# Optimization experiments

Measured on AMD Instinct MI355X. Metric: run time of the kernel, lower is better.

The kernel has to match this reference:

```python
import jax, jax.numpy as jnp
import numpy as np

K_RATIO = 0.7  # initial_ratio at epoch 0

def setup_inputs() -> dict:
    key = jax.random.key(0)
    k1, k2, k3 = jax.random.split(key, 3)
    B, D, C = 65536, 512, 1000
    features = jax.random.normal(k1, (B, D), dtype=jnp.float32)
    targets = jax.random.randint(k2, (B,), 0, C, dtype=jnp.int64)
    W = jax.random.normal(k3, (D, C), dtype=jnp.float32) / np.sqrt(D)
    b = jnp.zeros((C,), dtype=jnp.float32)
    return {"features": features, "targets": targets, "W": W, "b": b}

def reference(features, targets, W, b):
    # model: linear classifier -> logits [B, C]
    logits = features @ W + b
    # per-sample cross-entropy (reduction='none')
    logp = jax.nn.log_softmax(logits, axis=-1)
    losses = -jnp.take_along_axis(logp, targets[:, None], axis=-1)[:, 0]  # [B]
    B = features.shape[0]
    num_ohem = int(B * K_RATIO)
    # top-k hard examples, mean of their losses
    top_vals, _ = jax.lax.top_k(losses, num_ohem)
    return top_vals.mean()
```

## Files before the change

### kernel.cpp

```cpp
#include <hip/hip_runtime.h>
#include <hip/hip_bf16.h>

#define BTOT 65536
#define DDIM 512
#define CDIM 1000
#define KSEL 45875

#define L2E 1.44269504088896340736f
#define LN2 0.69314718055994530942f
#define NEG_BIG -1.0e30f

typedef __attribute__((ext_vector_type(8))) short short8;
typedef __attribute__((ext_vector_type(8))) unsigned short ushort8;
typedef __attribute__((ext_vector_type(4))) float f32x4;

__device__ __forceinline__ unsigned short f2bf(float f) {
  unsigned u = __float_as_uint(f);
  u += 0x7FFFu + ((u >> 16) & 1u);
  return (unsigned short)(u >> 16);
}

__device__ __forceinline__ void gload_lds16(const void* g, void* l) {
  __builtin_amdgcn_global_load_lds(
      (const __attribute__((address_space(1))) unsigned int*)g,
      (__attribute__((address_space(3))) unsigned int*)l, 16, 0, 0);
}

__global__ void prep_wt(const float* __restrict__ W, unsigned short* __restrict__ Wg) {
  const int idx = blockIdx.x * 256 + threadIdx.x;
  const int c  = idx & 1023;
  const int k8 = idx >> 10;
  const int nc = c >> 5, cc = c & 31;
  ushort8 v;
#pragma unroll
  for (int j = 0; j < 8; ++j) {
    const int k = k8 * 8 + j;
    v[j] = (c < CDIM) ? f2bf(W[k * CDIM + c]) : (unsigned short)0;
  }
  const unsigned dst = (unsigned)nc * 32768u +
      (((((unsigned)cc) << 10) | (((unsigned)k8) << 4)) ^ ((((unsigned)cc) & 7u) << 4));
  *(ushort8*)((char*)Wg + dst) = v;
}

__global__ void prep_bias(const float* __restrict__ b, float* __restrict__ bp) {
  const int i = blockIdx.x * 256 + threadIdx.x;
  bp[i] = (i < CDIM) ? b[i] * L2E : NEG_BIG;
}

__global__ void zero_hist(unsigned* __restrict__ h) {
  ((uint4*)h)[blockIdx.x * 256 + threadIdx.x] = (uint4){0, 0, 0, 0};
}

__launch_bounds__(256, 2)
__global__ void ohem_losses(const float* __restrict__ feat,
                            const int* __restrict__ targets,
                            const unsigned short* __restrict__ Wg,
                            const float* __restrict__ bpad,
                            float* __restrict__ losses,
                            unsigned* __restrict__ histHi) {
  __shared__ unsigned char lbuf[2][32768];
  const int tid  = threadIdx.x;
  const int lane = tid & 63;
  const int wave = (blockIdx.x << 2) + (tid >> 6);
  const int rowB = wave << 5;
  const int l15  = lane & 15;
  const int lgrp = lane >> 4;

#pragma unroll
  for (int r = 0; r < 8; ++r) {
    const int off = (r * 256 + tid) * 16;
    gload_lds16((const char*)Wg + off, &lbuf[0][off]);
  }

  short8 a[2][16];
#pragma unroll
  for (int rf = 0; rf < 2; ++rf) {
    const float* src = feat + (size_t)(rowB + rf * 16 + l15) * DDIM + lgrp * 8;
#pragma unroll
    for (int ks = 0; ks < 16; ++ks) {
      const float4 f0 = *(const float4*)(src + ks * 32);
      const float4 f1 = *(const float4*)(src + ks * 32 + 4);
      short8 v;
      v[0] = (short)f2bf(f0.x); v[1] = (short)f2bf(f0.y);
      v[2] = (short)f2bf(f0.z); v[3] = (short)f2bf(f0.w);
      v[4] = (short)f2bf(f1.x); v[5] = (short)f2bf(f1.y);
      v[6] = (short)f2bf(f1.z); v[7] = (short)f2bf(f1.w);
      a[rf][ks] = v;
    }
  }

  int   tcol[8];
  float s[8], tv[8];
#pragma unroll
  for (int rf = 0; rf < 2; ++rf)
#pragma unroll
    for (int r = 0; r < 4; ++r) {
      const int slot = rf * 4 + r;
      tcol[slot] = targets[rowB + rf * 16 + lgrp * 4 + r];
      s[slot] = 0.f; tv[slot] = NEG_BIG;
    }

  __syncthreads();

  const unsigned xm    = ((unsigned)(l15 & 7)) << 4;
  const unsigned base0 = (((unsigned)l15) << 10) | (((unsigned)lgrp) << 4);
  const unsigned base1 = base0 + (16u << 10);

  for (int nc = 0; nc < 32; ++nc) {
    const int cur = nc & 1;
    if (nc + 1 < 32) {
      const char* src = (const char*)Wg + (size_t)(nc + 1) * 32768;
#pragma unroll
      for (int r = 0; r < 8; ++r) {
        const int off = (r * 256 + tid) * 16;
        gload_lds16(src + off, &lbuf[cur ^ 1][off]);
      }
    }

    f32x4 acc[2][2];
#pragma unroll
    for (int rf = 0; rf < 2; ++rf)
#pragma unroll
      for (int cf = 0; cf < 2; ++cf) acc[rf][cf] = (f32x4){0.f, 0.f, 0.f, 0.f};

    const unsigned char* lb = &lbuf[cur][0];
#pragma unroll
    for (int ks = 0; ks < 16; ++ks) {
      const unsigned o0 = (base0 | (((unsigned)ks) << 6)) ^ xm;
      const unsigned o1 = (base1 | (((unsigned)ks) << 6)) ^ xm;
      const short8 b0 = *(const short8*)(lb + o0);
      const short8 b1 = *(const short8*)(lb + o1);
      acc[0][0] = __builtin_amdgcn_mfma_f32_16x16x32_bf16(a[0][ks], b0, acc[0][0], 0, 0, 0);
      acc[0][1] = __builtin_amdgcn_mfma_f32_16x16x32_bf16(a[0][ks], b1, acc[0][1], 0, 0, 0);
      acc[1][0] = __builtin_amdgcn_mfma_f32_16x16x32_bf16(a[1][ks], b0, acc[1][0], 0, 0, 0);
      acc[1][1] = __builtin_amdgcn_mfma_f32_16x16x32_bf16(a[1][ks], b1, acc[1][1], 0, 0, 0);
    }

    const int col0 = (nc << 5) + l15;
    const int col1 = col0 + 16;
    const float bb0 = bpad[col0];
    const float bb1 = bpad[col1];
#pragma unroll
    for (int rf = 0; rf < 2; ++rf)
#pragma unroll
      for (int r = 0; r < 4; ++r) {
        const int slot = rf * 4 + r;
        const float z0 = fmaf(acc[rf][0][r], L2E, bb0);
        const float z1 = fmaf(acc[rf][1][r], L2E, bb1);
        if (col0 == tcol[slot]) tv[slot] = z0;
        if (col1 == tcol[slot]) tv[slot] = z1;
        s[slot] += __builtin_amdgcn_exp2f(z0) + __builtin_amdgcn_exp2f(z1);
      }

    __syncthreads();
  }

#pragma unroll
  for (int st = 1; st <= 8; st <<= 1)
#pragma unroll
    for (int slot = 0; slot < 8; ++slot) {
      s[slot] += __shfl_xor(s[slot], st, 64);
      tv[slot] = fmaxf(tv[slot], __shfl_xor(tv[slot], st, 64));
    }

  if (l15 == 0) {
#pragma unroll
    for (int rf = 0; rf < 2; ++rf)
#pragma unroll
      for (int r = 0; r < 4; ++r) {
        const int slot = rf * 4 + r;
        float loss = LN2 * (__builtin_amdgcn_logf(s[slot]) - tv[slot]);
        loss = fmaxf(loss, 0.f);
        losses[rowB + rf * 16 + lgrp * 4 + r] = loss;
        atomicAdd(&histHi[__float_as_uint(loss) >> 16], 1u);
      }
  }
}

__global__ void scan_level(const unsigned* __restrict__ hist,
                           unsigned* __restrict__ state, const int level) {
  const int t = threadIdx.x;
  __shared__ unsigned sh[256];
  const unsigned k       = (level == 0) ? (unsigned)KSEL : state[1];
  const unsigned oldpref = (level == 0) ? 0u : state[0];

  unsigned gs = 0;
  const uint4* hp = (const uint4*)(hist + t * 256);
#pragma unroll 4
  for (int i = 0; i < 64; ++i) { const uint4 h = hp[i]; gs += h.x + h.y + h.z + h.w; }
  sh[t] = gs;
  __syncthreads();
  for (int off = 1; off < 256; off <<= 1) {
    unsigned v = sh[t];
    if (t + off < 256) v += sh[t + off];
    __syncthreads();
    sh[t] = v;
    __syncthreads();
  }
  const unsigned incl  = sh[t];
  const unsigned above = (t < 255) ? sh[t + 1] : 0u;
  if (above < k && k <= incl) {
    unsigned kk = k - above;
    int b = 255;
    for (; b > 0; --b) {
      const unsigned c = hist[t * 256 + b];
      if (kk <= c) break;
      kk -= c;
    }
    const unsigned bin = (unsigned)(t * 256 + b);
    if (level == 0) { state[0] = bin << 16;      state[1] = kk; }
    else            { state[0] = oldpref | bin;  state[1] = kk; }
  }
}

__global__ void hist_lo(const float* __restrict__ losses,
                        const unsigned* __restrict__ state,
                        unsigned* __restrict__ hLo) {
  const unsigned pref = state[0] >> 16;
  const int i = blockIdx.x * 256 + threadIdx.x;
  const unsigned u = ((const unsigned*)losses)[i];
  if ((u >> 16) == pref) atomicAdd(&hLo[u & 0xFFFFu], 1u);
}

__global__ void ohem_sum(const float* __restrict__ losses,
                         const unsigned* __restrict__ state,
                         float* __restrict__ psum, unsigned* __restrict__ pcnt) {
  const unsigned ut = state[0];
  const int i = blockIdx.x * 256 + threadIdx.x;
  const float v = losses[i];
  const unsigned u = __float_as_uint(v);
  float    sv = (u > ut) ? v  : 0.f;
  unsigned sc = (u > ut) ? 1u : 0u;
#pragma unroll
  for (int st = 32; st >= 1; st >>= 1) {
    sv += __shfl_xor(sv, st, 64);
    sc += __shfl_xor(sc, st, 64);
  }
  __shared__ float    wsum[4];
  __shared__ unsigned wcnt[4];
  const int w = threadIdx.x >> 6;
  if ((threadIdx.x & 63) == 0) { wsum[w] = sv; wcnt[w] = sc; }
  __syncthreads();
  if (threadIdx.x == 0) {
    psum[blockIdx.x] = wsum[0] + wsum[1] + wsum[2] + wsum[3];
    pcnt[blockIdx.x] = wcnt[0] + wcnt[1] + wcnt[2] + wcnt[3];
  }
}

__global__ void ohem_final(const float* __restrict__ psum,
                           const unsigned* __restrict__ pcnt,
                           const unsigned* __restrict__ state,
                           float* __restrict__ out) {
  float    sv = psum[threadIdx.x];
  unsigned sc = pcnt[threadIdx.x];
#pragma unroll
  for (int st = 32; st >= 1; st >>= 1) {
    sv += __shfl_xor(sv, st, 64);
    sc += __shfl_xor(sc, st, 64);
  }
  __shared__ float    wsum[4];
  __shared__ unsigned wcnt[4];
  const int w = threadIdx.x >> 6;
  if ((threadIdx.x & 63) == 0) { wsum[w] = sv; wcnt[w] = sc; }
  __syncthreads();
  if (threadIdx.x == 0) {
    const float    sum = wsum[0] + wsum[1] + wsum[2] + wsum[3];
    const unsigned cnt = wcnt[0] + wcnt[1] + wcnt[2] + wcnt[3];
    const float t = __uint_as_float(state[0]);
    out[0] = (sum + (float)(KSEL - cnt) * t) / (float)KSEL;
  }
}

extern "C" void kernel_launch(void* const* d_in, const int* in_sizes, int n_in,
                              void* d_out, int out_size, void* d_ws, size_t ws_size,
                              hipStream_t stream) {
  const float* feat    = (const float*)d_in[0];
  const int*   targets = (const int*)d_in[1];
  const float* W       = (const float*)d_in[2];
  const float* b       = (const float*)d_in[3];
  float* out = (float*)d_out;

  char* ws = (char*)d_ws;
  unsigned short* Wg     = (unsigned short*)ws;
  float*          bp     = (float*)(ws + 1048576);
  float*          losses = (float*)(ws + 1052672);
  unsigned*       hHi    = (unsigned*)(ws + 1314816);
  unsigned*       hLo    = (unsigned*)(ws + 1576960);
  unsigned*       state  = (unsigned*)(ws + 1839104);
  float*          psum   = (float*)(ws + 1839360);
  unsigned*       pcnt   = (unsigned*)(ws + 1840384);

  zero_hist<<<128, 256, 0, stream>>>(hHi);
  prep_wt<<<256, 256, 0, stream>>>(W, Wg);
  prep_bias<<<4, 256, 0, stream>>>(b, bp);
  ohem_losses<<<512, 256, 0, stream>>>(feat, targets, Wg, bp, losses, hHi);
  scan_level<<<1, 256, 0, stream>>>(hHi, state, 0);
  hist_lo<<<256, 256, 0, stream>>>(losses, state, hLo);
  scan_level<<<1, 256, 0, stream>>>(hLo, state, 1);
  ohem_sum<<<256, 256, 0, stream>>>(losses, state, psum, pcnt);
  ohem_final<<<1, 256, 0, stream>>>(psum, pcnt, state, out);
}
```

Before: 288.7 us.

## Split classes across blocks with a resident 128-column weight panel in LDS

Restructures the fused GEMM+softmax kernel so each block keeps a 128-class slice of the bf16 weights resident in 128KB of LDS and streams 2048 feature rows through it. Partial exp-sums and target logits go to per-panel buffers that a new combine kernel reduces into losses and the histogram. This drops the per-chunk weight streaming and barriers, but the features are now read eight times. The three prep kernels are also merged into one launch, and the function attribute is set on every call.

Result: slower. 621.8 us (+115.4%).

```diff
diff --git a/kernel.cpp b/kernel.cpp
--- a/kernel.cpp
+++ b/kernel.cpp
@@ -20,161 +20,153 @@
   return (unsigned short)(u >> 16);
 }
 
+__device__ __forceinline__ unsigned pk2bf(float lo, float hi) {
+  __hip_bfloat162 h = __float22bfloat162_rn(float2{lo, hi});
+  return *(unsigned*)&h;
+}
+
 __device__ __forceinline__ void gload_lds16(const void* g, void* l) {
   __builtin_amdgcn_global_load_lds(
       (const __attribute__((address_space(1))) unsigned int*)g,
       (__attribute__((address_space(3))) unsigned int*)l, 16, 0, 0);
 }
 
-__global__ void prep_wt(const float* __restrict__ W, unsigned short* __restrict__ Wg) {
-  const int idx = blockIdx.x * 256 + threadIdx.x;
-  const int c  = idx & 1023;
-  const int k8 = idx >> 10;
-  const int nc = c >> 5, cc = c & 31;
-  ushort8 v;
-#pragma unroll
-  for (int j = 0; j < 8; ++j) {
-    const int k = k8 * 8 + j;
-    v[j] = (c < CDIM) ? f2bf(W[k * CDIM + c]) : (unsigned short)0;
-  }
-  const unsigned dst = (unsigned)nc * 32768u +
-      (((((unsigned)cc) << 10) | (((unsigned)k8) << 4)) ^ ((((unsigned)cc) & 7u) << 4));
-  *(ushort8*)((char*)Wg + dst) = v;
-}
-
-__global__ void prep_bias(const float* __restrict__ b, float* __restrict__ bp) {
-  const int i = blockIdx.x * 256 + threadIdx.x;
-  bp[i] = (i < CDIM) ? b[i] * L2E : NEG_BIG;
-}
-
-__global__ void zero_hist(unsigned* __restrict__ h) {
-  ((uint4*)h)[blockIdx.x * 256 + threadIdx.x] = (uint4){0, 0, 0, 0};
-}
-
-__launch_bounds__(256, 2)
+__global__ void prep_all(const float* __restrict__ W, const float* __restrict__ b,
+                         unsigned short* __restrict__ Wg, float* __restrict__ bp,
+                         unsigned* __restrict__ hzero) {
+  const int bid = blockIdx.x, tid = threadIdx.x;
+  if (bid < 256) {
+    const int idx = bid * 256 + tid;
+    const int c  = idx & 1023;
+    const int k8 = idx >> 10;
+    const int p = c >> 7, cl = c & 127;
+    ushort8 v;
+#pragma unroll
+    for (int j = 0; j < 8; ++j) {
+      const int k = k8 * 8 + j;
+      v[j] = (c < CDIM) ? f2bf(W[k * CDIM + c]) : (unsigned short)0;
+    }
+    const unsigned off = ((((unsigned)cl) << 10) | (((unsigned)k8) << 4)) ^
+                         ((((unsigned)cl) & 7u) << 4);
+    *(ushort8*)((char*)Wg + (size_t)p * 131072 + off) = v;
+  } else if (bid < 384) {
+    ((uint4*)hzero)[(bid - 256) * 256 + tid] = (uint4){0, 0, 0, 0};
+  } else {
+    for (int i = tid; i < 1024; i += 256) bp[i] = (i < CDIM) ? b[i] * L2E : NEG_BIG;
+  }
+}
+
+__launch_bounds__(512, 2)
 __global__ void ohem_losses(const float* __restrict__ feat,
                             const int* __restrict__ targets,
                             const unsigned short* __restrict__ Wg,
                             const float* __restrict__ bpad,
-                            float* __restrict__ losses,
-                            unsigned* __restrict__ histHi) {
-  __shared__ unsigned char lbuf[2][32768];
-  const int tid  = threadIdx.x;
-  const int lane = tid & 63;
-  const int wave = (blockIdx.x << 2) + (tid >> 6);
-  const int rowB = wave << 5;
-  const int l15  = lane & 15;
-  const int lgrp = lane >> 4;
-
-#pragma unroll
-  for (int r = 0; r < 8; ++r) {
-    const int off = (r * 256 + tid) * 16;
-    gload_lds16((const char*)Wg + off, &lbuf[0][off]);
-  }
-
-  short8 a[2][16];
-#pragma unroll
-  for (int rf = 0; rf < 2; ++rf) {
-    const float* src = feat + (size_t)(rowB + rf * 16 + l15) * DDIM + lgrp * 8;
+                            float* __restrict__ spart,
+                            float* __restrict__ tvpart) {
+  extern __shared__ char lbuf[];
+  const int tid = threadIdx.x, lane = tid & 63, w = tid >> 6;
+  const int l15 = lane & 15, lgrp = lane >> 4;
+  const int bid = blockIdx.x;
+  const int xcd = bid & 7, q = bid >> 3;
+  const int p = q & 7, stp8 = q >> 3;
+  const int gs = xcd * 4 + stp8;
+  const int rowS = gs << 11;
+
+  const char* src = (const char*)Wg + (size_t)p * 131072;
+#pragma unroll
+  for (int r = 0; r < 16; ++r) {
+    const int off = (r * 512 + tid) * 16;
+    gload_lds16(src + off, lbuf + off);
+  }
+
+  const int p128 = p << 7;
+  float bb[8]; int colc[8];
+#pragma unroll
+  for (int cf = 0; cf < 8; ++cf) {
+    colc[cf] = p128 + cf * 16 + l15;
+    bb[cf] = bpad[colc[cf]];
+  }
+
+  __syncthreads();
+
+  const unsigned xm   = ((unsigned)(l15 & 7)) << 4;
+  const unsigned bofs = (((unsigned)l15) << 10) | (((unsigned)lgrp) << 4);
+
+  for (int it = 0; it < 8; ++it) {
+    const int rowB = rowS + (it << 8) + (w << 5);
+    const float* a0 = feat + (size_t)(rowB + l15) * DDIM + lgrp * 8;
+
+    f32x4 acc[2][8];
+#pragma unroll
+    for (int g = 0; g < 2; ++g)
+#pragma unroll
+      for (int cf = 0; cf < 8; ++cf) acc[g][cf] = (f32x4){0.f, 0.f, 0.f, 0.f};
+
 #pragma unroll
     for (int ks = 0; ks < 16; ++ks) {
-      const float4 f0 = *(const float4*)(src + ks * 32);
-      const float4 f1 = *(const float4*)(src + ks * 32 + 4);
-      short8 v;
-      v[0] = (short)f2bf(f0.x); v[1] = (short)f2bf(f0.y);
-      v[2] = (short)f2bf(f0.z); v[3] = (short)f2bf(f0.w);
-      v[4] = (short)f2bf(f1.x); v[5] = (short)f2bf(f1.y);
-      v[6] = (short)f2bf(f1.z); v[7] = (short)f2bf(f1.w);
-      a[rf][ks] = v;
-    }
-  }
-
-  int   tcol[8];
-  float s[8], tv[8];
-#pragma unroll
-  for (int rf = 0; rf < 2; ++rf)
-#pragma unroll
-    for (int r = 0; r < 4; ++r) {
-      const int slot = rf * 4 + r;
-      tcol[slot] = targets[rowB + rf * 16 + lgrp * 4 + r];
-      s[slot] = 0.f; tv[slot] = NEG_BIG;
-    }
-
-  __syncthreads();
-
-  const unsigned xm    = ((unsigned)(l15 & 7)) << 4;
-  const unsigned base0 = (((unsigned)l15) << 10) | (((unsigned)lgrp) << 4);
-  const unsigned base1 = base0 + (16u << 10);
-
-  for (int nc = 0; nc < 32; ++nc) {
-    const int cur = nc & 1;
-    if (nc + 1 < 32) {
-      const char* src = (const char*)Wg + (size_t)(nc + 1) * 32768;
-#pragma unroll
-      for (int r = 0; r < 8; ++r) {
-        const int off = (r * 256 + tid) * 16;
-        gload_lds16(src + off, &lbuf[cur ^ 1][off]);
+      short8 ag[2];
+#pragma unroll
+      for (int g = 0; g < 2; ++g) {
+        const float* ap = a0 + g * (16 * DDIM) + ks * 32;
+        const float4 f0 = *(const float4*)ap;
+        const float4 f1 = *(const float4*)(ap + 4);
+        union { unsigned u[4]; short8 s; } cv;
+        cv.u[0] = pk2bf(f0.x, f0.y);
+        cv.u[1] = pk2bf(f0.z, f0.w);
+        cv.u[2] = pk2bf(f1.x, f1.y);
+        cv.u[3] = pk2bf(f1.z, f1.w);
+        ag[g] = cv.s;
+      }
+      const unsigned kb = (bofs + ((unsigned)ks << 6)) ^ xm;
+#pragma unroll
+      for (int cf = 0; cf < 8; ++cf) {
+        const short8 bfr = *(const short8*)(lbuf + kb + (unsigned)cf * 16384u);
+        acc[0][cf] = __builtin_amdgcn_mfma_f32_16x16x32_bf16(ag[0], bfr, acc[0][cf], 0, 0, 0);
+        acc[1][cf] = __builtin_amdgcn_mfma_f32_16x16x32_bf16(ag[1], bfr, acc[1][cf], 0, 0, 0);
       }
     }
 
-    f32x4 acc[2][2];
-#pragma unroll
-    for (int rf = 0; rf < 2; ++rf)
-#pragma unroll
-      for (int cf = 0; cf < 2; ++cf) acc[rf][cf] = (f32x4){0.f, 0.f, 0.f, 0.f};
-
-    const unsigned char* lb = &lbuf[cur][0];
-#pragma unroll
-    for (int ks = 0; ks < 16; ++ks) {
-      const unsigned o0 = (base0 | (((unsigned)ks) << 6)) ^ xm;
-      const unsigned o1 = (base1 | (((unsigned)ks) << 6)) ^ xm;
-      const short8 b0 = *(const short8*)(lb + o0);
-      const short8 b1 = *(const short8*)(lb + o1);
-      acc[0][0] = __builtin_amdgcn_mfma_f32_16x16x32_bf16(a[0][ks], b0, acc[0][0], 0, 0, 0);
-      acc[0][1] = __builtin_amdgcn_mfma_f32_16x16x32_bf16(a[0][ks], b1, acc[0][1], 0, 0, 0);
-      acc[1][0] = __builtin_amdgcn_mfma_f32_16x16x32_bf16(a[1][ks], b0, acc[1][0], 0, 0, 0);
-      acc[1][1] = __builtin_amdgcn_mfma_f32_16x16x32_bf16(a[1][ks], b1, acc[1][1], 0, 0, 0);
-    }
-
-    const int col0 = (nc << 5) + l15;
-    const int col1 = col0 + 16;
-    const float bb0 = bpad[col0];
-    const float bb1 = bpad[col1];
-#pragma unroll
-    for (int rf = 0; rf < 2; ++rf)
+#pragma unroll
+    for (int g = 0; g < 2; ++g)
 #pragma unroll
       for (int r = 0; r < 4; ++r) {
-        const int slot = rf * 4 + r;
-        const float z0 = fmaf(acc[rf][0][r], L2E, bb0);
-        const float z1 = fmaf(acc[rf][1][r], L2E, bb1);
-        if (col0 == tcol[slot]) tv[slot] = z0;
-        if (col1 == tcol[slot]) tv[slot] = z1;
-        s[slot] += __builtin_amdgcn_exp2f(z0) + __builtin_amdgcn_exp2f(z1);
+        const int row = rowB + g * 16 + lgrp * 4 + r;
+        const int tc = targets[row];
+        float s = 0.f, tv = NEG_BIG;
+#pragma unroll
+        for (int cf = 0; cf < 8; ++cf) {
+          const float z = fmaf(acc[g][cf][r], L2E, bb[cf]);
+          if (colc[cf] == tc) tv = z;
+          s += __builtin_amdgcn_exp2f(z);
+        }
+#pragma unroll
+        for (int st = 1; st <= 8; st <<= 1) {
+          s += __shfl_xor(s, st, 64);
+          tv = fmaxf(tv, __shfl_xor(tv, st, 64));
+        }
+        if (l15 == 0) {
+          spart[(size_t)p * BTOT + row]  = s;
+          tvpart[(size_t)p * BTOT + row] = tv;
+        }
       }
-
-    __syncthreads();
-  }
-
-#pragma unroll
-  for (int st = 1; st <= 8; st <<= 1)
-#pragma unroll
-    for (int slot = 0; slot < 8; ++slot) {
-      s[slot] += __shfl_xor(s[slot], st, 64);
-      tv[slot] = fmaxf(tv[slot], __shfl_xor(tv[slot], st, 64));
-    }
-
-  if (l15 == 0) {
-#pragma unroll
-    for (int rf = 0; rf < 2; ++rf)
-#pragma unroll
-      for (int r = 0; r < 4; ++r) {
-        const int slot = rf * 4 + r;
-        float loss = LN2 * (__builtin_amdgcn_logf(s[slot]) - tv[slot]);
-        loss = fmaxf(loss, 0.f);
-        losses[rowB + rf * 16 + lgrp * 4 + r] = loss;
-        atomicAdd(&histHi[__float_as_uint(loss) >> 16], 1u);
-      }
-  }
+  }
+}
+
+__global__ void combine_hist(const float* __restrict__ spart,
+                             const float* __restrict__ tvpart,
+                             float* __restrict__ losses,
+                             unsigned* __restrict__ hHi) {
+  const int row = blockIdx.x * 256 + threadIdx.x;
+  float s = 0.f, tv = NEG_BIG;
+#pragma unroll
+  for (int p = 0; p < 8; ++p) {
+    s  += spart[(size_t)p * BTOT + row];
+    tv  = fmaxf(tv, tvpart[(size_t)p * BTOT + row]);
+  }
+  float loss = LN2 * (__builtin_amdgcn_logf(s) - tv);
+  loss = fmaxf(loss, 0.f);
+  losses[row] = loss;
+  atomicAdd(&hHi[__float_as_uint(loss) >> 16], 1u);
 }
 
 __global__ void scan_level(const unsigned* __restrict__ hist,
@@ -201,13 +193,13 @@
   const unsigned above = (t < 255) ? sh[t + 1] : 0u;
   if (above < k && k <= incl) {
     unsigned kk = k - above;
-    int b = 255;
-    for (; b > 0; --b) {
-      const unsigned c = hist[t * 256 + b];
+    int bkt = 255;
+    for (; bkt > 0; --bkt) {
+      const unsigned c = hist[t * 256 + bkt];
       if (kk <= c) break;
       kk -= c;
     }
-    const unsigned bin = (unsigned)(t * 256 + b);
+    const unsigned bin = (unsigned)(t * 256 + bkt);
     if (level == 0) { state[0] = bin << 16;      state[1] = kk; }
     else            { state[0] = oldpref | bin;  state[1] = kk; }
   }
@@ -283,17 +275,21 @@
   char* ws = (char*)d_ws;
   unsigned short* Wg     = (unsigned short*)ws;
   float*          bp     = (float*)(ws + 1048576);
-  float*          losses = (float*)(ws + 1052672);
-  unsigned*       hHi    = (unsigned*)(ws + 1314816);
-  unsigned*       hLo    = (unsigned*)(ws + 1576960);
-  unsigned*       state  = (unsigned*)(ws + 1839104);
-  float*          psum   = (float*)(ws + 1839360);
-  unsigned*       pcnt   = (unsigned*)(ws + 1840384);
-
-  zero_hist<<<128, 256, 0, stream>>>(hHi);
-  prep_wt<<<256, 256, 0, stream>>>(W, Wg);
-  prep_bias<<<4, 256, 0, stream>>>(b, bp);
-  ohem_losses<<<512, 256, 0, stream>>>(feat, targets, Wg, bp, losses, hHi);
+  float*          spart  = (float*)(ws + 1052672);
+  float*          tvpart = (float*)(ws + 3149824);
+  float*          losses = (float*)(ws + 5246976);
+  unsigned*       hHi    = (unsigned*)(ws + 5509120);
+  unsigned*       hLo    = (unsigned*)(ws + 5771264);
+  unsigned*       state  = (unsigned*)(ws + 6033408);
+  float*          psum   = (float*)(ws + 6033664);
+  unsigned*       pcnt   = (unsigned*)(ws + 6034688);
+
+  hipFuncSetAttribute((const void*)ohem_losses,
+                      hipFuncAttributeMaxDynamicSharedMemorySize, 131072);
+
+  prep_all<<<385, 256, 0, stream>>>(W, b, Wg, bp, hHi);
+  ohem_losses<<<256, 512, 131072, stream>>>(feat, targets, Wg, bp, spart, tvpart);
+  combine_hist<<<256, 256, 0, stream>>>(spart, tvpart, losses, hHi);
   scan_level<<<1, 256, 0, stream>>>(hHi, state, 0);
   hist_lo<<<256, 256, 0, stream>>>(losses, state, hLo);
   scan_level<<<1, 256, 0, stream>>>(hLo, state, 1);
```

## Shrink loss-kernel tiles to 16-column chunks with 128-thread blocks; fuse prep kernels

Applied to the files above, without the earlier changes.

The three prep kernels (weight conversion, bias padding, histogram zeroing) are merged into one launch. The weight chunk layout changes from 32 to 16 columns per chunk. The main loss kernel now uses 128-thread blocks of 2 waves, 16 KB LDS double buffers and 64 column iterations, with bias cached in LDS. The aim is more resident blocks and better latency hiding through smaller LDS use. The cost is twice as many barrier-synchronised iterations and half as many MFMAs per B-fragment load, which lowers reuse of each LDS read.

Measured after the change: 343.0 us. +18.8%, slower.

```diff
diff --git a/kernel.cpp b/kernel.cpp
--- a/kernel.cpp
+++ b/kernel.cpp
@@ -20,56 +20,66 @@
   return (unsigned short)(u >> 16);
 }
 
+__device__ __forceinline__ short8 cvt8(const float4 f0, const float4 f1) {
+  short8 v;
+  v[0] = (short)f2bf(f0.x); v[1] = (short)f2bf(f0.y);
+  v[2] = (short)f2bf(f0.z); v[3] = (short)f2bf(f0.w);
+  v[4] = (short)f2bf(f1.x); v[5] = (short)f2bf(f1.y);
+  v[6] = (short)f2bf(f1.z); v[7] = (short)f2bf(f1.w);
+  return v;
+}
+
 __device__ __forceinline__ void gload_lds16(const void* g, void* l) {
   __builtin_amdgcn_global_load_lds(
       (const __attribute__((address_space(1))) unsigned int*)g,
       (__attribute__((address_space(3))) unsigned int*)l, 16, 0, 0);
 }
 
-__global__ void prep_wt(const float* __restrict__ W, unsigned short* __restrict__ Wg) {
-  const int idx = blockIdx.x * 256 + threadIdx.x;
-  const int c  = idx & 1023;
-  const int k8 = idx >> 10;
-  const int nc = c >> 5, cc = c & 31;
-  ushort8 v;
-#pragma unroll
-  for (int j = 0; j < 8; ++j) {
-    const int k = k8 * 8 + j;
-    v[j] = (c < CDIM) ? f2bf(W[k * CDIM + c]) : (unsigned short)0;
-  }
-  const unsigned dst = (unsigned)nc * 32768u +
-      (((((unsigned)cc) << 10) | (((unsigned)k8) << 4)) ^ ((((unsigned)cc) & 7u) << 4));
-  *(ushort8*)((char*)Wg + dst) = v;
-}
-
-__global__ void prep_bias(const float* __restrict__ b, float* __restrict__ bp) {
-  const int i = blockIdx.x * 256 + threadIdx.x;
-  bp[i] = (i < CDIM) ? b[i] * L2E : NEG_BIG;
-}
-
-__global__ void zero_hist(unsigned* __restrict__ h) {
-  ((uint4*)h)[blockIdx.x * 256 + threadIdx.x] = (uint4){0, 0, 0, 0};
-}
-
-__launch_bounds__(256, 2)
+__global__ void prep_all(const float* __restrict__ W, const float* __restrict__ b,
+                         unsigned short* __restrict__ Wg, float* __restrict__ bp,
+                         unsigned* __restrict__ hzero) {
+  const int bid = blockIdx.x, tid = threadIdx.x;
+  if (bid < 256) {
+    const int idx = bid * 256 + tid;
+    const int c  = idx & 1023;
+    const int k8 = idx >> 10;
+    const int p = c >> 4, cc = c & 15;
+    ushort8 v;
+#pragma unroll
+    for (int j = 0; j < 8; ++j) {
+      const int k = k8 * 8 + j;
+      v[j] = (c < CDIM) ? f2bf(W[k * CDIM + c]) : (unsigned short)0;
+    }
+    const unsigned off = ((((unsigned)cc) << 10) | (((unsigned)k8) << 4)) ^
+                         ((((unsigned)cc) & 7u) << 4);
+    *(ushort8*)((char*)Wg + (size_t)p * 16384 + off) = v;
+  } else if (bid < 384) {
+    ((uint4*)hzero)[(bid - 256) * 256 + tid] = (uint4){0, 0, 0, 0};
+  } else {
+    for (int i = tid; i < 1024; i += 256) bp[i] = (i < CDIM) ? b[i] * L2E : NEG_BIG;
+  }
+}
+
+__launch_bounds__(128)
 __global__ void ohem_losses(const float* __restrict__ feat,
                             const int* __restrict__ targets,
                             const unsigned short* __restrict__ Wg,
                             const float* __restrict__ bpad,
                             float* __restrict__ losses,
                             unsigned* __restrict__ histHi) {
-  __shared__ unsigned char lbuf[2][32768];
-  const int tid  = threadIdx.x;
-  const int lane = tid & 63;
-  const int wave = (blockIdx.x << 2) + (tid >> 6);
-  const int rowB = wave << 5;
-  const int l15  = lane & 15;
-  const int lgrp = lane >> 4;
+  __shared__ char lbuf[2][16384];
+  __shared__ float biasLds[1024];
+  const int tid = threadIdx.x, lane = tid & 63, w = tid >> 6;
+  const int l15 = lane & 15, lgrp = lane >> 4;
+  const int rowB = blockIdx.x * 64 + w * 32;
+
+#pragma unroll
+  for (int j = 0; j < 8; ++j) biasLds[tid * 8 + j] = bpad[tid * 8 + j];
 
 #pragma unroll
   for (int r = 0; r < 8; ++r) {
-    const int off = (r * 256 + tid) * 16;
-    gload_lds16((const char*)Wg + off, &lbuf[0][off]);
+    const int off = (r * 128 + tid) * 16;
+    gload_lds16((const char*)Wg + off, &lbuf[0][0] + off);
   }
 
   short8 a[2][16];
@@ -80,12 +90,7 @@
     for (int ks = 0; ks < 16; ++ks) {
       const float4 f0 = *(const float4*)(src + ks * 32);
       const float4 f1 = *(const float4*)(src + ks * 32 + 4);
-      short8 v;
-      v[0] = (short)f2bf(f0.x); v[1] = (short)f2bf(f0.y);
-      v[2] = (short)f2bf(f0.z); v[3] = (short)f2bf(f0.w);
-      v[4] = (short)f2bf(f1.x); v[5] = (short)f2bf(f1.y);
-      v[6] = (short)f2bf(f1.z); v[7] = (short)f2bf(f1.w);
-      a[rf][ks] = v;
+      a[rf][ks] = cvt8(f0, f1);
     }
   }
 
@@ -102,55 +107,41 @@
 
   __syncthreads();
 
-  const unsigned xm    = ((unsigned)(l15 & 7)) << 4;
-  const unsigned base0 = (((unsigned)l15) << 10) | (((unsigned)lgrp) << 4);
-  const unsigned base1 = base0 + (16u << 10);
-
-  for (int nc = 0; nc < 32; ++nc) {
+  const unsigned xm   = ((unsigned)(l15 & 7)) << 4;
+  const unsigned bofs = (((unsigned)l15) << 10) | (((unsigned)lgrp) << 4);
+
+  for (int nc = 0; nc < 64; ++nc) {
     const int cur = nc & 1;
-    if (nc + 1 < 32) {
-      const char* src = (const char*)Wg + (size_t)(nc + 1) * 32768;
+    if (nc + 1 < 64) {
+      const char* src = (const char*)Wg + (size_t)(nc + 1) * 16384;
 #pragma unroll
       for (int r = 0; r < 8; ++r) {
-        const int off = (r * 256 + tid) * 16;
-        gload_lds16(src + off, &lbuf[cur ^ 1][off]);
+        const int off = (r * 128 + tid) * 16;
+        gload_lds16(src + off, &lbuf[cur ^ 1][0] + off);
       }
     }
 
-    f32x4 acc[2][2];
-#pragma unroll
-    for (int rf = 0; rf < 2; ++rf)
-#pragma unroll
-      for (int cf = 0; cf < 2; ++cf) acc[rf][cf] = (f32x4){0.f, 0.f, 0.f, 0.f};
-
-    const unsigned char* lb = &lbuf[cur][0];
+    f32x4 acc0 = (f32x4){0.f, 0.f, 0.f, 0.f};
+    f32x4 acc1 = (f32x4){0.f, 0.f, 0.f, 0.f};
+    const char* lb = &lbuf[cur][0];
 #pragma unroll
     for (int ks = 0; ks < 16; ++ks) {
-      const unsigned o0 = (base0 | (((unsigned)ks) << 6)) ^ xm;
-      const unsigned o1 = (base1 | (((unsigned)ks) << 6)) ^ xm;
-      const short8 b0 = *(const short8*)(lb + o0);
-      const short8 b1 = *(const short8*)(lb + o1);
-      acc[0][0] = __builtin_amdgcn_mfma_f32_16x16x32_bf16(a[0][ks], b0, acc[0][0], 0, 0, 0);
-      acc[0][1] = __builtin_amdgcn_mfma_f32_16x16x32_bf16(a[0][ks], b1, acc[0][1], 0, 0, 0);
-      acc[1][0] = __builtin_amdgcn_mfma_f32_16x16x32_bf16(a[1][ks], b0, acc[1][0], 0, 0, 0);
-      acc[1][1] = __builtin_amdgcn_mfma_f32_16x16x32_bf16(a[1][ks], b1, acc[1][1], 0, 0, 0);
-    }
-
-    const int col0 = (nc << 5) + l15;
-    const int col1 = col0 + 16;
-    const float bb0 = bpad[col0];
-    const float bb1 = bpad[col1];
-#pragma unroll
-    for (int rf = 0; rf < 2; ++rf)
-#pragma unroll
-      for (int r = 0; r < 4; ++r) {
-        const int slot = rf * 4 + r;
-        const float z0 = fmaf(acc[rf][0][r], L2E, bb0);
-        const float z1 = fmaf(acc[rf][1][r], L2E, bb1);
-        if (col0 == tcol[slot]) tv[slot] = z0;
-        if (col1 == tcol[slot]) tv[slot] = z1;
-        s[slot] += __builtin_amdgcn_exp2f(z0) + __builtin_amdgcn_exp2f(z1);
-      }
+      const short8 b0 = *(const short8*)(lb + ((bofs | ((unsigned)ks << 6)) ^ xm));
+      acc0 = __builtin_amdgcn_mfma_f32_16x16x32_bf16(a[0][ks], b0, acc0, 0, 0, 0);
+      acc1 = __builtin_amdgcn_mfma_f32_16x16x32_bf16(a[1][ks], b0, acc1, 0, 0, 0);
+    }
+
+    const int col0 = (nc << 4) + l15;
+    const float bb0 = biasLds[col0];
+#pragma unroll
+    for (int r = 0; r < 4; ++r) {
+      const float z0 = fmaf(acc0[r], L2E, bb0);
+      const float z1 = fmaf(acc1[r], L2E, bb0);
+      if (col0 == tcol[r])     tv[r]     = z0;
+      if (col0 == tcol[4 + r]) tv[4 + r] = z1;
+      s[r]     += __builtin_amdgcn_exp2f(z0);
+      s[4 + r] += __builtin_amdgcn_exp2f(z1);
+    }
 
     __syncthreads();
   }
@@ -177,6 +168,7 @@
   }
 }
 
+
 __global__ void scan_level(const unsigned* __restrict__ hist,
                            unsigned* __restrict__ state, const int level) {
   const int t = threadIdx.x;
@@ -201,13 +193,13 @@
   const unsigned above = (t < 255) ? sh[t + 1] : 0u;
   if (above < k && k <= incl) {
     unsigned kk = k - above;
-    int b = 255;
-    for (; b > 0; --b) {
-      const unsigned c = hist[t * 256 + b];
+    int bkt = 255;
+    for (; bkt > 0; --bkt) {
+      const unsigned c = hist[t * 256 + bkt];
       if (kk <= c) break;
       kk -= c;
     }
-    const unsigned bin = (unsigned)(t * 256 + b);
+    const unsigned bin = (unsigned)(t * 256 + bkt);
     if (level == 0) { state[0] = bin << 16;      state[1] = kk; }
     else            { state[0] = oldpref | bin;  state[1] = kk; }
   }
@@ -290,10 +282,8 @@
   float*          psum   = (float*)(ws + 1839360);
   unsigned*       pcnt   = (unsigned*)(ws + 1840384);
 
-  zero_hist<<<128, 256, 0, stream>>>(hHi);
-  prep_wt<<<256, 256, 0, stream>>>(W, Wg);
-  prep_bias<<<4, 256, 0, stream>>>(b, bp);
-  ohem_losses<<<512, 256, 0, stream>>>(feat, targets, Wg, bp, losses, hHi);
+  prep_all<<<385, 256, 0, stream>>>(W, b, Wg, bp, hHi);
+  ohem_losses<<<1024, 128, 0, stream>>>(feat, targets, Wg, bp, losses, hHi);
   scan_level<<<1, 256, 0, stream>>>(hHi, state, 0);
   hist_lo<<<256, 256, 0, stream>>>(losses, state, hLo);
   scan_level<<<1, 256, 0, stream>>>(hLo, state, 1);
```
